# Optimization experiments

Hardware: AMD Instinct MI355X
Metric: run time of the kernel (lower is better)

Reference implementation:

```python
import jax, jax.numpy as jnp
import numpy as np

N = 100000   # nodes
E = 1600000  # edges
G = 1024     # graphs
V = 51       # attr_dims[0]+1 embedding rows (padding_idx=0)
EMB = 32
H = 2        # heads
D = 64       # hidden_dim (per-head out channels)
DC = H * D   # 128 = dim_conv
NEG_GAT = 0.2   # PyG GATConv default negative_slope
NEG_ACT = 0.05  # module's leaky_relu slope
LN_EPS = 1e-5


def setup_inputs() -> dict:
    key = jax.random.key(0)
    ks = jax.random.split(key, 20)
    def nrm(k, shape, scale=0.1):
        return jax.random.normal(k, shape, dtype=jnp.float32) * scale
    x = jax.random.randint(ks[0], (N, 1), 0, V)
    edge_index = jax.random.randint(ks[1], (2, E), 0, N)
    batch_idx = jnp.sort(jax.random.randint(ks[2], (N,), 0, G))
    return {
        'x': x, 'edge_index': edge_index, 'batch_idx': batch_idx,
        'emb': nrm(ks[3], (V, EMB)).at[0].set(0.0),  # padding_idx=0
        'ln_g': jnp.ones((EMB,), jnp.float32), 'ln_b': jnp.zeros((EMB,), jnp.float32),
        'W1': nrm(ks[4], (EMB, DC)), 'a_src1': nrm(ks[5], (H, D)), 'a_dst1': nrm(ks[6], (H, D)), 'b1': nrm(ks[7], (DC,)),
        'W2': nrm(ks[8], (DC, DC)), 'a_src2': nrm(ks[9], (H, D)), 'a_dst2': nrm(ks[10], (H, D)), 'b2': nrm(ks[11], (DC,)),
        'gw1': nrm(ks[12], (DC, D)), 'gb1': nrm(ks[13], (D,)),
        'gw2': nrm(ks[14], (D, 1)), 'gb2': nrm(ks[15], (1,)),
    }


def _gat_conv(xf, src, dst, W, a_src, a_dst, b):
    # xf: [N, in]; returns [N, H*D]. PyG GATConv, eval mode (attn dropout off).
    xw = (xf @ W).reshape(N, H, D)                           # [N,H,D]
    al_s = jnp.einsum('nhd,hd->nh', xw, a_src)
    al_d = jnp.einsum('nhd,hd->nh', xw, a_dst)
    e = jax.nn.leaky_relu(al_s[src] + al_d[dst], NEG_GAT)    # [E',H]
    m = jax.ops.segment_max(e, dst, num_segments=N)
    ex = jnp.exp(e - m[dst])
    s = jax.ops.segment_sum(ex, dst, num_segments=N)
    alpha = ex / s[dst]                                      # segment softmax over incoming edges
    msg = xw[src] * alpha[:, :, None]                        # [E',H,D]
    out = jax.ops.segment_sum(msg, dst, num_segments=N)      # [N,H,D]
    return out.reshape(N, DC) + b


def reference(x, edge_index, batch_idx, emb, ln_g, ln_b,
              W1, a_src1, a_dst1, b1, W2, a_src2, a_dst2, b2,
              gw1, gb1, gw2, gb2):
    # embedding + LayerNorm (dropout off in eval)
    xe = emb[x[:, 0]]                                        # [N,32]
    mu = jnp.mean(xe, axis=-1, keepdims=True)
    var = jnp.var(xe, axis=-1, keepdims=True)
    xe = (xe - mu) * jax.lax.rsqrt(var + LN_EPS) * ln_g + ln_b
    # add self loops (GATConv add_self_loops=True)
    ar = jnp.arange(N, dtype=edge_index.dtype)
    src = jnp.concatenate([edge_index[0], ar])
    dst = jnp.concatenate([edge_index[1], ar])
    h = jax.nn.leaky_relu(_gat_conv(xe, src, dst, W1, a_src1, a_dst1, b1), NEG_ACT)
    h = _gat_conv(h, src, dst, W2, a_src2, a_dst2, b2)       # [N,128]
    # attentional aggregation over graphs
    gate = jax.nn.leaky_relu(h @ gw1 + gb1, NEG_ACT) @ gw2 + gb2   # [N,1]
    gm = jax.ops.segment_max(gate, batch_idx, num_segments=G)
    ge = jnp.exp(gate - gm[batch_idx])
    gs = jax.ops.segment_sum(ge, batch_idx, num_segments=G)
    w = ge / gs[batch_idx]
    z = jax.ops.segment_sum(w * h, batch_idx, num_segments=G)      # [G,128]
    return h, z
```

## Files before the change

kernel.cpp:

```cpp
#include <hip/hip_runtime.h>
#include <hip/hip_bf16.h>
#include <stdint.h>

typedef unsigned short u16;
typedef unsigned int   u32;
typedef __attribute__((ext_vector_type(8))) short bf16x8;
typedef __attribute__((ext_vector_type(4))) float f32x4;

#define NEG_GAT 0.2f
#define NEG_ACT 0.05f
#define LN_EPS  1e-5f
#define NPARAM  15

__device__ __forceinline__ float bf2f(u32 bits16){
  union { u32 u; float f; } v; v.u = bits16 << 16; return v.f;
}
__device__ __forceinline__ u16 f2bf(float f){
  union { float f; u32 u; } v; v.f = f;
  u32 u = v.u;
  u32 r = (u + 0x7fffu + ((u >> 16) & 1u)) >> 16;
  return (u16)r;
}
__device__ __forceinline__ float lrelu(float x, float s){ return fmaxf(x, s * x); }

__device__ __forceinline__ int geti(const int* __restrict__ p, int i, int enc){
  return p[enc ? (2 * i) : i];
}


struct CvtParams {
  const void* src[NPARAM];
  float*      dst[NPARAM];
  int         n[NPARAM];
};

#define MAXB  2048

__global__ void k_detect(const u32* __restrict__ ln_g_raw, const int* __restrict__ ei_raw,
                         int* __restrict__ flags, int* __restrict__ bcnt)
{
  const int t = threadIdx.x;
  for (int i = t; i < MAXB; i += 256) bcnt[i] = 0;
  if (t == 0){
    flags[0] = (ln_g_raw[0] == 0x3F800000u) ? 0 : 1;
    int zeros = 0;
    for (int j = 0; j < 64; j++) if (ei_raw[2 * j + 1] == 0) zeros++;
    flags[1] = (zeros >= 60) ? 1 : 0;
    flags[2] = 0;
    flags[3] = 0;
  }
}

__global__ void k_convert(CvtParams P, const int* __restrict__ flag)
{
  const int pi  = blockIdx.y;
  const int idx = blockIdx.x * 256 + threadIdx.x;
  if (idx >= P.n[pi]) return;
  if (*flag == 0) P.dst[pi][idx] = ((const float*)P.src[pi])[idx];
  else            P.dst[pi][idx] = bf2f(((const u16*)P.src[pi])[idx]);
}


__global__ void k_checks(const int* __restrict__ batch, const int* __restrict__ x,
                         const int* __restrict__ iflag,
                         int n, int V, int* __restrict__ errflag)
{
  int i = blockIdx.x * 256 + threadIdx.x;
  const int enc = *iflag;
  if (i < n){
    int v = geti(x, i, enc);
    if ((unsigned)v >= (unsigned)V) atomicOr(errflag, 16);
    if (i < n - 1 && geti(batch, i, enc) > geti(batch, i + 1, enc)) atomicOr(errflag, 8);
  }
}

__global__ void k_check_edges(const int* __restrict__ ei, const int* __restrict__ iflag,
                              int E, int n, int* __restrict__ errflag)
{
  int e = blockIdx.x * 256 + threadIdx.x;
  if (e < E){
    int enc = *iflag;
    int s = geti(ei, e, enc);
    int d = geti(ei, E + e, enc);
    if ((unsigned)s >= (unsigned)n || (unsigned)d >= (unsigned)n) atomicOr(errflag, 32);
  }
}


__global__ void k_hist(const int* __restrict__ ei, const int* __restrict__ iflag,
                       int* __restrict__ counts, int E, int n)
{
  int e = blockIdx.x * 256 + threadIdx.x;
  if (e < E){
    int d = geti(ei, E + e, *iflag);
    d = min(max(d, 0), n - 1);
    atomicAdd(&counts[d], 1);
  }
}

__global__ void k_scanA(const int* __restrict__ counts, int* __restrict__ rowptr,
                        int* __restrict__ bsums, int n)
{
  __shared__ int sd[1024];
  int tid = threadIdx.x;
  int gid = blockIdx.x * 1024 + tid;
  int v = (gid < n) ? counts[gid] : 0;
  sd[tid] = v;
  __syncthreads();
  for (int off = 1; off < 1024; off <<= 1){
    int t = 0;
    if (tid >= off) t = sd[tid - off];
    __syncthreads();
    if (tid >= off) sd[tid] += t;
    __syncthreads();
  }
  if (gid < n) rowptr[gid] = sd[tid] - v;
  if (tid == 1023) bsums[blockIdx.x] = sd[1023];
}

__global__ void k_scanB(const int* __restrict__ bsums, int* __restrict__ boffs, int nb)
{
  __shared__ int sd[128];
  int tid = threadIdx.x;
  int v = (tid < nb) ? bsums[tid] : 0;
  sd[tid] = v;
  __syncthreads();
  for (int off = 1; off < 128; off <<= 1){
    int t = 0;
    if (tid >= off) t = sd[tid - off];
    __syncthreads();
    if (tid >= off) sd[tid] += t;
    __syncthreads();
  }
  if (tid < nb) boffs[tid] = sd[tid] - v;
}

__global__ void k_scanC(int* __restrict__ rowptr, const int* __restrict__ boffs,
                        int* __restrict__ cursor, int n, int Etot)
{
  int gid = blockIdx.x * 1024 + threadIdx.x;
  if (gid < n){
    int v = rowptr[gid] + boffs[blockIdx.x];
    rowptr[gid] = v;
    cursor[gid] = v;
  }
  if (gid == 0) rowptr[n] = Etot;
}

__global__ void k_scatter(const int* __restrict__ ei, const int* __restrict__ iflag,
                          int* __restrict__ cursor, int* __restrict__ csr, int E, int n)
{
  int e = blockIdx.x * 256 + threadIdx.x;
  if (e < E){
    int enc = *iflag;
    int s = geti(ei, e, enc);
    int d = geti(ei, E + e, enc);
    d = min(max(d, 0), n - 1);
    int pos = atomicAdd(&cursor[d], 1);
    csr[pos] = s;
  }
}

__global__ void k_check_rows(const int* __restrict__ rowptr, const int* __restrict__ cursor,
                             int n, int* __restrict__ errflag)
{
  int i = blockIdx.x * 256 + threadIdx.x;
  if (i < n){
    if (cursor[i] != rowptr[i + 1]) atomicOr(errflag, 1);
    if (i == 0 && rowptr[0] != 0)   atomicOr(errflag, 4);
  }
}

__global__ void k_check_csr(const int* __restrict__ csr, int E, int n, int* __restrict__ errflag)
{
  int e = blockIdx.x * 256 + threadIdx.x;
  if (e < E && (unsigned)csr[e] >= (unsigned)n) atomicOr(errflag, 2);
}


#define BSH   9
#define BSZ   512
#define BMSK  511
#define BINB  8192
#define BTH   512

__global__ void k_bhist(const int* __restrict__ ei, const int* __restrict__ iflag,
                        int* __restrict__ bcnt, int E, int N, int nbuck)
{
  __shared__ int h[MAXB];
  const int t = threadIdx.x;
  for (int i = t; i < nbuck; i += 256) h[i] = 0;
  __syncthreads();
  const int enc = *iflag;
  for (int e = blockIdx.x * 256 + t; e < E; e += gridDim.x * 256){
    int d = geti(ei, E + e, enc);
    d = min(max(d, 0), N - 1);
    atomicAdd(&h[d >> BSH], 1);
  }
  __syncthreads();
  for (int i = t; i < nbuck; i += 256){
    int c = h[i];
    if (c) atomicAdd(&bcnt[i], c);
  }
}

__global__ void k_bscan(const int* __restrict__ bcnt, int* __restrict__ boff,
                        int* __restrict__ gcur, int* __restrict__ rowptr,
                        int nbuck, int N, int E)
{
  __shared__ int sd[MAXB];
  const int lane = threadIdx.x;
  for (int i = lane; i < nbuck; i += 64) sd[i] = bcnt[i];
  __syncthreads();
  const int L = (nbuck + 63) >> 6;
  const int b0 = lane * L;
  int sum = 0;
  for (int j = 0; j < L; j++){ int idx = b0 + j; if (idx < nbuck) sum += sd[idx]; }
  int excl = sum;
  for (int off = 1; off < 64; off <<= 1){
    int x = __shfl_up(excl, off);
    if (lane >= off) excl += x;
  }
  excl -= sum;
  int run = excl;
  for (int j = 0; j < L; j++){
    int idx = b0 + j;
    if (idx < nbuck){ boff[idx] = run; gcur[idx] = run; run += sd[idx]; }
  }
  if (lane == 0){ boff[nbuck] = E; rowptr[N] = E; }
}

__global__ __launch_bounds__(BTH) void k_bbin(
    const int* __restrict__ ei, const int* __restrict__ iflag,
    int* __restrict__ gcur, u32* __restrict__ binned,
    int E, int N, int nbuck, int* __restrict__ errflag)
{
  __shared__ u32 stage[BINB];
  __shared__ u16 sbk[BINB];
  __shared__ int hist[MAXB];
  __shared__ int base[MAXB];
  __shared__ int gpos[MAXB];
  const int t   = threadIdx.x;
  const int e0  = blockIdx.x * BINB;
  const int cnt = min(BINB, E - e0);
  const int enc = *iflag;

  for (int i = t; i < nbuck; i += BTH) hist[i] = 0;
  __syncthreads();

  u32 pv[16]; int bk[16]; int rk[16];
  int bad = 0;
  #pragma unroll
  for (int k = 0; k < 16; k++){
    bk[k] = -1;
    int lo = k * BTH + t;
    if (lo < cnt){
      int e = e0 + lo;
      int s = geti(ei, e, enc);
      int d = geti(ei, E + e, enc);
      if ((unsigned)s >= (unsigned)N || (unsigned)d >= (unsigned)N) bad = 1;
      s = min(max(s, 0), N - 1);
      d = min(max(d, 0), N - 1);
      int b = d >> BSH;
      pv[k] = ((u32)s << BSH) | (u32)(d & BMSK);
      bk[k] = b;
      rk[k] = atomicAdd(&hist[b], 1);
    }
  }
  if (bad) atomicOr(errflag, 32);
  __syncthreads();

  if (t < 64){
    const int L = (nbuck + 63) >> 6;
    const int b0 = t * L;
    int sum = 0;
    for (int j = 0; j < L; j++){ int idx = b0 + j; if (idx < nbuck) sum += hist[idx]; }
    int excl = sum;
    for (int off = 1; off < 64; off <<= 1){
      int x = __shfl_up(excl, off);
      if (t >= off) excl += x;
    }
    excl -= sum;
    int run = excl;
    for (int j = 0; j < L; j++){
      int idx = b0 + j;
      if (idx < nbuck){ base[idx] = run; run += hist[idx]; }
    }
  }
  __syncthreads();

  for (int i = t; i < nbuck; i += BTH){
    int c = hist[i];
    gpos[i] = c ? atomicAdd(&gcur[i], c) : 0;
  }
  __syncthreads();

  #pragma unroll
  for (int k = 0; k < 16; k++){
    if (bk[k] >= 0){
      int slot = base[bk[k]] + rk[k];
      stage[slot] = pv[k];
      sbk[slot]   = (u16)bk[k];
    }
  }
  __syncthreads();

  for (int j = t; j < cnt; j += BTH){
    int b = sbk[j];
    binned[gpos[b] + (j - base[b])] = stage[j];
  }
}

__global__ __launch_bounds__(256) void k_bcsr(
    const u32* __restrict__ binned, const int* __restrict__ boff,
    int* __restrict__ rowptr, int* __restrict__ csr, int N, int nbuck)
{
  __shared__ int cnt[BSZ];
  __shared__ int rp[BSZ];
  __shared__ int cur[BSZ];
  const int b = blockIdx.x;
  const int t = threadIdx.x;
  const int lo = boff[b], hi = boff[b + 1];

  for (int i = t; i < BSZ; i += 256){ cnt[i] = 0; cur[i] = 0; }
  __syncthreads();

  for (int j = lo + t; j < hi; j += 256)
    atomicAdd(&cnt[binned[j] & BMSK], 1);
  __syncthreads();

  if (t < 64){
    const int b0 = t * 8;
    int sum = 0;
    #pragma unroll
    for (int j = 0; j < 8; j++) sum += cnt[b0 + j];
    int excl = sum;
    for (int off = 1; off < 64; off <<= 1){
      int x = __shfl_up(excl, off);
      if (t >= off) excl += x;
    }
    excl -= sum;
    int run = excl;
    #pragma unroll
    for (int j = 0; j < 8; j++){ rp[b0 + j] = run; run += cnt[b0 + j]; }
  }
  __syncthreads();

  const int node0 = b << BSH;
  for (int i = t; i < BSZ; i += 256){
    int node = node0 + i;
    if (node < N) rowptr[node] = lo + rp[i];
  }

  for (int j = lo + t; j < hi; j += 256){
    u32 pvv = binned[j];
    int dl  = pvv & BMSK;
    int pos = lo + rp[dl] + atomicAdd(&cur[dl], 1);
    csr[pos] = (int)(pvv >> BSH);
  }
}


__global__ void k_stamp_if(const int* __restrict__ errflag, float* __restrict__ out, int nel)
{
  int f = *errflag;
  if (f == 0) return;
  float s = 500.0f + 100.0f * (float)f;
  int i = blockIdx.x * 256 + threadIdx.x;
  if (i < nel) out[i] = s;
}

__global__ void k_stamp(float* __restrict__ out, int nel, float val)
{
  int i = blockIdx.x * 256 + threadIdx.x;
  if (i < nel) out[i] = val;
}


__global__ __launch_bounds__(128) void k_tables(
    const float* __restrict__ emb,
    const float* __restrict__ ln_g, const float* __restrict__ ln_b,
    const float* __restrict__ W1, const float* __restrict__ a_src,
    const float* __restrict__ a_dst,
    const float* __restrict__ W2, const float* __restrict__ gw1,
    int V,
    u16* __restrict__ xwv, float* __restrict__ alsv, float* __restrict__ aldv,
    u16* __restrict__ pb2, u16* __restrict__ pbg)
{
  const int bid = blockIdx.x;
  const int t   = threadIdx.x;

  if (bid >= V){
    if (t >= 64) return;
    int pw = bid - V;
    const float* W; int ncols, ntiles, blk; u16* pb;
    if (pw < 32){ W = W2; ncols = 128; ntiles = 8; blk = pw;      pb = pb2; }
    else        { W = gw1; ncols = 64;  ntiles = 4; blk = pw - 32; pb = pbg; }
    const int ktile = blk / ntiles;
    const int ntile = blk % ntiles;
    const int n  = ntile * 16 + (t & 15);
    const int k0 = ktile * 32 + (t >> 4) * 8;
    u16* dst = pb + ((size_t)blk * 64 + t) * 8;
    #pragma unroll
    for (int j = 0; j < 8; j++)
      dst[j] = f2bf(W[(k0 + j) * ncols + n]);
    return;
  }

  __shared__ float se[32];
  __shared__ float stats[2];
  __shared__ float sxw[128];
  const int v = bid;
  if (t < 32) se[t] = emb[v * 32 + t];
  __syncthreads();
  if (t == 0){
    float s1 = 0.f, s2 = 0.f;
    for (int k = 0; k < 32; k++){ s1 += se[k]; s2 += se[k] * se[k]; }
    float mu = s1 * (1.f / 32.f);
    float var = s2 * (1.f / 32.f) - mu * mu;
    stats[0] = mu; stats[1] = rsqrtf(var + LN_EPS);
  }
  __syncthreads();
  const float mu = stats[0], rs = stats[1];
  float o = 0.f;
  for (int k = 0; k < 32; k++){
    float xe = (se[k] - mu) * rs * ln_g[k] + ln_b[k];
    o += xe * W1[k * 128 + t];
  }
  sxw[t] = o;
  xwv[v * 128 + t] = f2bf(o);
  __syncthreads();
  if (t < 2){
    float ps = 0.f, pd = 0.f;
    for (int d = 0; d < 64; d++){
      float vv = sxw[t * 64 + d];
      ps += vv * a_src[t * 64 + d];
      pd += vv * a_dst[t * 64 + d];
    }
    alsv[2 * v + t] = ps;
    aldv[2 * v + t] = pd;
  }
}


__global__ __launch_bounds__(256, 4) void k_gatw1(
    const int* __restrict__ rowptr, const int* __restrict__ csr,
    const int* __restrict__ x, const int* __restrict__ iflag,
    const float* __restrict__ alsv, const float* __restrict__ aldv,
    const u16* __restrict__ xwv, const float* __restrict__ bias,
    int N, int V, float* __restrict__ out)
{
  extern __shared__ char smem[];
  u16*    sxwv  = (u16*)smem;
  float2* sals  = (float2*)(smem + (size_t)V * 256);
  float2* sald  = sals + V;
  float4* sedge = (float4*)(smem + (size_t)V * 256 + (size_t)V * 16);

  const int tid = threadIdx.x;
  const int enc = *iflag;

  {
    const uint4* gx = (const uint4*)xwv;
    uint4* lx = (uint4*)sxwv;
    for (int idx = tid; idx < V * 16; idx += 256) lx[idx] = gx[idx];
    const float2* ga = (const float2*)alsv;
    const float2* gd = (const float2*)aldv;
    for (int idx = tid; idx < V; idx += 256){ sals[idx] = ga[idx]; sald[idx] = gd[idx]; }
  }
  __syncthreads();

  const int wave = tid >> 6;
  const int lane = tid & 63;
  const int sub  = lane >> 4;
  const int c16  = lane & 15;
  float4* mst = sedge + wave * 64;

  for (int i = blockIdx.x * 4 + wave; i < N; i += gridDim.x * 4){
    const int r0 = rowptr[i], deg = rowptr[i + 1] - r0, total = deg + 1;
    int vi = geti(x, i, enc); vi = min(max(vi, 0), V - 1);
    const float2 ad = sald[vi];

    float sum0 = 0.f, sum1 = 0.f;
    float acc[8];
    #pragma unroll
    for (int r = 0; r < 8; r++) acc[r] = 0.f;

    if (total <= 64){
      int vs = vi;
      float a0 = -3.0e38f, a1 = -3.0e38f;
      if (lane < total){
        int s = (lane < deg) ? csr[r0 + lane] : i;
        int v = geti(x, s, enc);
        vs = min(max(v, 0), V - 1);
        float2 as = sals[vs];
        a0 = lrelu(as.x + ad.x, NEG_GAT);
        a1 = lrelu(as.y + ad.y, NEG_GAT);
      }
      float m0 = a0, m1 = a1;
      #pragma unroll
      for (int off = 32; off; off >>= 1){
        m0 = fmaxf(m0, __shfl_xor(m0, off));
        m1 = fmaxf(m1, __shfl_xor(m1, off));
      }
      float ex0 = 0.f, ex1 = 0.f;
      if (lane < total){ ex0 = __expf(a0 - m0); ex1 = __expf(a1 - m1); }
      sum0 = ex0; sum1 = ex1;
      mst[lane] = make_float4(__int_as_float(vs), ex0, ex1, 0.f);
      int qmax = (total + 3) & ~3;
      for (int q = 0; q < qmax; q += 4){
        float4 md = mst[q + sub];
        int   vj = __float_as_int(md.x);
        float ej = (c16 < 8) ? md.y : md.z;
        uint4 w = *(const uint4*)(sxwv + vj * 128 + c16 * 8);
        acc[0] += ej * bf2f(w.x & 0xffffu); acc[1] += ej * bf2f(w.x >> 16);
        acc[2] += ej * bf2f(w.y & 0xffffu); acc[3] += ej * bf2f(w.y >> 16);
        acc[4] += ej * bf2f(w.z & 0xffffu); acc[5] += ej * bf2f(w.z >> 16);
        acc[6] += ej * bf2f(w.w & 0xffffu); acc[7] += ej * bf2f(w.w >> 16);
      }
    } else {
      float m0 = -3.0e38f, m1 = -3.0e38f;
      for (int k = lane; k < total; k += 64){
        int s = (k < deg) ? csr[r0 + k] : i;
        int v = geti(x, s, enc); v = min(max(v, 0), V - 1);
        float2 as = sals[v];
        m0 = fmaxf(m0, lrelu(as.x + ad.x, NEG_GAT));
        m1 = fmaxf(m1, lrelu(as.y + ad.y, NEG_GAT));
      }
      #pragma unroll
      for (int off = 32; off; off >>= 1){
        m0 = fmaxf(m0, __shfl_xor(m0, off));
        m1 = fmaxf(m1, __shfl_xor(m1, off));
      }
      for (int base = 0; base < total; base += 64){
        int k = base + lane;
        int vs = vi; float ex0 = 0.f, ex1 = 0.f;
        if (k < total){
          int s = (k < deg) ? csr[r0 + k] : i;
          int v = geti(x, s, enc); vs = min(max(v, 0), V - 1);
          float2 as = sals[vs];
          ex0 = __expf(lrelu(as.x + ad.x, NEG_GAT) - m0);
          ex1 = __expf(lrelu(as.y + ad.y, NEG_GAT) - m1);
        }
        sum0 += ex0; sum1 += ex1;
        mst[lane] = make_float4(__int_as_float(vs), ex0, ex1, 0.f);
        int cnt = min(64, total - base);
        int qmax = (cnt + 3) & ~3;
        for (int q = 0; q < qmax; q += 4){
          float4 md = mst[q + sub];
          int   vj = __float_as_int(md.x);
          float ej = (c16 < 8) ? md.y : md.z;
          uint4 w = *(const uint4*)(sxwv + vj * 128 + c16 * 8);
          acc[0] += ej * bf2f(w.x & 0xffffu); acc[1] += ej * bf2f(w.x >> 16);
          acc[2] += ej * bf2f(w.y & 0xffffu); acc[3] += ej * bf2f(w.y >> 16);
          acc[4] += ej * bf2f(w.z & 0xffffu); acc[5] += ej * bf2f(w.z >> 16);
          acc[6] += ej * bf2f(w.w & 0xffffu); acc[7] += ej * bf2f(w.w >> 16);
        }
      }
    }

    #pragma unroll
    for (int off = 32; off; off >>= 1){
      sum0 += __shfl_xor(sum0, off);
      sum1 += __shfl_xor(sum1, off);
    }
    #pragma unroll
    for (int r = 0; r < 8; r++){
      acc[r] += __shfl_xor(acc[r], 16);
      acc[r] += __shfl_xor(acc[r], 32);
    }

    if (sub == 0){
      float inv = 1.f / ((c16 < 8) ? sum0 : sum1);
      const float4* bp = (const float4*)(bias + c16 * 8);
      float4 b0 = bp[0], b1 = bp[1];
      float4 o0, o1;
      o0.x = lrelu(acc[0] * inv + b0.x, NEG_ACT); o0.y = lrelu(acc[1] * inv + b0.y, NEG_ACT);
      o0.z = lrelu(acc[2] * inv + b0.z, NEG_ACT); o0.w = lrelu(acc[3] * inv + b0.w, NEG_ACT);
      o1.x = lrelu(acc[4] * inv + b1.x, NEG_ACT); o1.y = lrelu(acc[5] * inv + b1.y, NEG_ACT);
      o1.z = lrelu(acc[6] * inv + b1.z, NEG_ACT); o1.w = lrelu(acc[7] * inv + b1.w, NEG_ACT);
      float* op = out + (size_t)i * 128 + c16 * 8;
      *(float4*)op       = o0;
      *(float4*)(op + 4) = o1;
    }
  }
}

__global__ __launch_bounds__(64, 8) void k_gatw1g(
    const int* __restrict__ rowptr, const int* __restrict__ csr,
    const int* __restrict__ x, const int* __restrict__ iflag,
    const float* __restrict__ alsv, const float* __restrict__ aldv,
    const u16* __restrict__ xwv, const float* __restrict__ bias,
    int V, float* __restrict__ out)
{
  const int i    = blockIdx.x;
  const int lane = threadIdx.x;
  const int sub  = lane >> 4;
  const int c16  = lane & 15;
  const int enc  = *iflag;
  const int r0 = rowptr[i], deg = rowptr[i + 1] - r0, total = deg + 1;
  int vi = geti(x, i, enc); vi = min(max(vi, 0), V - 1);
  const float ad0 = aldv[2 * vi], ad1 = aldv[2 * vi + 1];

  float sum0 = 0.f, sum1 = 0.f;
  float acc[8];
  #pragma unroll
  for (int r = 0; r < 8; r++) acc[r] = 0.f;

  float m0 = -3.0e38f, m1 = -3.0e38f;
  for (int k = lane; k < total; k += 64){
    int s = (k < deg) ? csr[r0 + k] : i;
    int v = geti(x, s, enc); v = min(max(v, 0), V - 1);
    float2 as = *(const float2*)(alsv + 2 * v);
    m0 = fmaxf(m0, lrelu(as.x + ad0, NEG_GAT));
    m1 = fmaxf(m1, lrelu(as.y + ad1, NEG_GAT));
  }
  #pragma unroll
  for (int off = 32; off; off >>= 1){
    m0 = fmaxf(m0, __shfl_xor(m0, off));
    m1 = fmaxf(m1, __shfl_xor(m1, off));
  }
  for (int base = 0; base < total; base += 64){
    int k = base + lane;
    int vs = vi; float ex0 = 0.f, ex1 = 0.f;
    if (k < total){
      int s = (k < deg) ? csr[r0 + k] : i;
      int v = geti(x, s, enc); vs = min(max(v, 0), V - 1);
      float2 as = *(const float2*)(alsv + 2 * vs);
      ex0 = __expf(lrelu(as.x + ad0, NEG_GAT) - m0);
      ex1 = __expf(lrelu(as.y + ad1, NEG_GAT) - m1);
    }
    sum0 += ex0; sum1 += ex1;
    int cnt = min(64, total - base);
    int qmax = (cnt + 3) & ~3;
    for (int q = 0; q < qmax; q += 4){
      int   j  = q + sub;
      int   vj = __shfl(vs, j);
      float e0 = __shfl(ex0, j);
      float e1 = __shfl(ex1, j);
      float ej = (c16 < 8) ? e0 : e1;
      uint4 w = *(const uint4*)(xwv + (size_t)vj * 128 + c16 * 8);
      acc[0] += ej * bf2f(w.x & 0xffffu); acc[1] += ej * bf2f(w.x >> 16);
      acc[2] += ej * bf2f(w.y & 0xffffu); acc[3] += ej * bf2f(w.y >> 16);
      acc[4] += ej * bf2f(w.z & 0xffffu); acc[5] += ej * bf2f(w.z >> 16);
      acc[6] += ej * bf2f(w.w & 0xffffu); acc[7] += ej * bf2f(w.w >> 16);
    }
  }

  #pragma unroll
  for (int off = 32; off; off >>= 1){
    sum0 += __shfl_xor(sum0, off);
    sum1 += __shfl_xor(sum1, off);
  }
  #pragma unroll
  for (int r = 0; r < 8; r++){
    acc[r] += __shfl_xor(acc[r], 16);
    acc[r] += __shfl_xor(acc[r], 32);
  }

  if (sub == 0){
    float inv = 1.f / ((c16 < 8) ? sum0 : sum1);
    const float4* bp = (const float4*)(bias + c16 * 8);
    float4 b0 = bp[0], b1 = bp[1];
    float4 o0, o1;
    o0.x = lrelu(acc[0] * inv + b0.x, NEG_ACT); o0.y = lrelu(acc[1] * inv + b0.y, NEG_ACT);
    o0.z = lrelu(acc[2] * inv + b0.z, NEG_ACT); o0.w = lrelu(acc[3] * inv + b0.w, NEG_ACT);
    o1.x = lrelu(acc[4] * inv + b1.x, NEG_ACT); o1.y = lrelu(acc[5] * inv + b1.y, NEG_ACT);
    o1.z = lrelu(acc[6] * inv + b1.z, NEG_ACT); o1.w = lrelu(acc[7] * inv + b1.w, NEG_ACT);
    float* op = out + (size_t)i * 128 + c16 * 8;
    *(float4*)op       = o0;
    *(float4*)(op + 4) = o1;
  }
}


__global__ __launch_bounds__(64, 8) void k_gatw2(
    const int* __restrict__ rowptr, const int* __restrict__ csr,
    const float* __restrict__ al_s, const float* __restrict__ al_d,
    const u16* __restrict__ xw, const float* __restrict__ bias,
    int apply_act, float* __restrict__ out)
{
  const int i    = blockIdx.x;
  const int lane = threadIdx.x;
  const int sub  = lane >> 4;
  const int c16  = lane & 15;
  const int r0 = rowptr[i], deg = rowptr[i + 1] - r0, total = deg + 1;
  const float2 ad = *(const float2*)(al_d + 2 * i);

  float sum0 = 0.f, sum1 = 0.f;
  float acc[8];
  #pragma unroll
  for (int r = 0; r < 8; r++) acc[r] = 0.f;

  if (total <= 64){
    int s = i;
    float a0 = -3.0e38f, a1 = -3.0e38f;
    if (lane < total){
      s = (lane < deg) ? csr[r0 + lane] : i;
      float2 as = *(const float2*)(al_s + 2 * s);
      a0 = lrelu(as.x + ad.x, NEG_GAT);
      a1 = lrelu(as.y + ad.y, NEG_GAT);
    }
    float m0 = a0, m1 = a1;
    #pragma unroll
    for (int off = 32; off; off >>= 1){
      m0 = fmaxf(m0, __shfl_xor(m0, off));
      m1 = fmaxf(m1, __shfl_xor(m1, off));
    }
    float ex0 = 0.f, ex1 = 0.f;
    if (lane < total){ ex0 = __expf(a0 - m0); ex1 = __expf(a1 - m1); }
    sum0 = ex0; sum1 = ex1;
    int qmax = (total + 3) & ~3;
    for (int q = 0; q < qmax; q += 4){
      int   j  = q + sub;
      int   sj = __shfl(s, j);
      float e0 = __shfl(ex0, j);
      float e1 = __shfl(ex1, j);
      float ej = (c16 < 8) ? e0 : e1;
      uint4 w = *(const uint4*)(xw + (size_t)sj * 128 + c16 * 8);
      acc[0] += ej * bf2f(w.x & 0xffffu); acc[1] += ej * bf2f(w.x >> 16);
      acc[2] += ej * bf2f(w.y & 0xffffu); acc[3] += ej * bf2f(w.y >> 16);
      acc[4] += ej * bf2f(w.z & 0xffffu); acc[5] += ej * bf2f(w.z >> 16);
      acc[6] += ej * bf2f(w.w & 0xffffu); acc[7] += ej * bf2f(w.w >> 16);
    }
  } else {
    float m0 = -3.0e38f, m1 = -3.0e38f;
    for (int k = lane; k < total; k += 64){
      int s = (k < deg) ? csr[r0 + k] : i;
      float2 as = *(const float2*)(al_s + 2 * s);
      m0 = fmaxf(m0, lrelu(as.x + ad.x, NEG_GAT));
      m1 = fmaxf(m1, lrelu(as.y + ad.y, NEG_GAT));
    }
    #pragma unroll
    for (int off = 32; off; off >>= 1){
      m0 = fmaxf(m0, __shfl_xor(m0, off));
      m1 = fmaxf(m1, __shfl_xor(m1, off));
    }
    for (int base = 0; base < total; base += 64){
      int k = base + lane;
      int s = i; float ex0 = 0.f, ex1 = 0.f;
      if (k < total){
        s = (k < deg) ? csr[r0 + k] : i;
        float2 as = *(const float2*)(al_s + 2 * s);
        ex0 = __expf(lrelu(as.x + ad.x, NEG_GAT) - m0);
        ex1 = __expf(lrelu(as.y + ad.y, NEG_GAT) - m1);
      }
      sum0 += ex0; sum1 += ex1;
      int cnt = min(64, total - base);
      int qmax = (cnt + 3) & ~3;
      for (int q = 0; q < qmax; q += 4){
        int   j  = q + sub;
        int   sj = __shfl(s, j);
        float e0 = __shfl(ex0, j);
        float e1 = __shfl(ex1, j);
        float ej = (c16 < 8) ? e0 : e1;
        uint4 w = *(const uint4*)(xw + (size_t)sj * 128 + c16 * 8);
        acc[0] += ej * bf2f(w.x & 0xffffu); acc[1] += ej * bf2f(w.x >> 16);
        acc[2] += ej * bf2f(w.y & 0xffffu); acc[3] += ej * bf2f(w.y >> 16);
        acc[4] += ej * bf2f(w.z & 0xffffu); acc[5] += ej * bf2f(w.z >> 16);
        acc[6] += ej * bf2f(w.w & 0xffffu); acc[7] += ej * bf2f(w.w >> 16);
      }
    }
  }

  #pragma unroll
  for (int off = 32; off; off >>= 1){
    sum0 += __shfl_xor(sum0, off);
    sum1 += __shfl_xor(sum1, off);
  }
  #pragma unroll
  for (int r = 0; r < 8; r++){
    acc[r] += __shfl_xor(acc[r], 16);
    acc[r] += __shfl_xor(acc[r], 32);
  }

  if (sub == 0){
    float inv = 1.f / ((c16 < 8) ? sum0 : sum1);
    const float4* bp = (const float4*)(bias + c16 * 8);
    float4 b0 = bp[0], b1 = bp[1];
    float4 o0, o1;
    o0.x = acc[0] * inv + b0.x; o0.y = acc[1] * inv + b0.y;
    o0.z = acc[2] * inv + b0.z; o0.w = acc[3] * inv + b0.w;
    o1.x = acc[4] * inv + b1.x; o1.y = acc[5] * inv + b1.y;
    o1.z = acc[6] * inv + b1.z; o1.w = acc[7] * inv + b1.w;
    if (apply_act){
      o0.x = lrelu(o0.x, NEG_ACT); o0.y = lrelu(o0.y, NEG_ACT);
      o0.z = lrelu(o0.z, NEG_ACT); o0.w = lrelu(o0.w, NEG_ACT);
      o1.x = lrelu(o1.x, NEG_ACT); o1.y = lrelu(o1.y, NEG_ACT);
      o1.z = lrelu(o1.z, NEG_ACT); o1.w = lrelu(o1.w, NEG_ACT);
    }
    float* op = out + (size_t)i * 128 + c16 * 8;
    *(float4*)op       = o0;
    *(float4*)(op + 4) = o1;
  }
}


__global__ __launch_bounds__(256, 2) void k_node2m(
    const float* __restrict__ h1, const u16* __restrict__ pb2,
    const float* __restrict__ a_src, const float* __restrict__ a_dst,
    int N, u16* __restrict__ xw, float* __restrict__ al_s, float* __restrict__ al_d)
{
  const int wave = threadIdx.x >> 6;
  const int lane = threadIdx.x & 63;
  const int rowbase = blockIdx.x * 64 + wave * 16;
  const int m    = lane & 15;
  const int quad = lane >> 4;

  int arow = rowbase + m; if (arow >= N) arow = N - 1;
  const float* aptr = h1 + (size_t)arow * 128 + quad * 8;

  f32x4 acc[8];
  #pragma unroll
  for (int nt = 0; nt < 8; nt++) acc[nt] = (f32x4){0.f, 0.f, 0.f, 0.f};

  #pragma unroll
  for (int kt = 0; kt < 4; kt++){
    float4 a0 = *(const float4*)(aptr + kt * 32);
    float4 a1 = *(const float4*)(aptr + kt * 32 + 4);
    bf16x8 af;
    af[0] = (short)f2bf(a0.x); af[1] = (short)f2bf(a0.y);
    af[2] = (short)f2bf(a0.z); af[3] = (short)f2bf(a0.w);
    af[4] = (short)f2bf(a1.x); af[5] = (short)f2bf(a1.y);
    af[6] = (short)f2bf(a1.z); af[7] = (short)f2bf(a1.w);
    const u16* bbase = pb2 + (((size_t)kt * 8) * 64 + lane) * 8;
    #pragma unroll
    for (int nt = 0; nt < 8; nt++){
      bf16x8 bf = *(const bf16x8*)(bbase + (size_t)nt * 64 * 8);
      acc[nt] = __builtin_amdgcn_mfma_f32_16x16x32_bf16(af, bf, acc[nt], 0, 0, 0);
    }
  }

  float asv[8], adv[8];
  #pragma unroll
  for (int nt = 0; nt < 8; nt++){
    asv[nt] = a_src[nt * 16 + m];
    adv[nt] = a_dst[nt * 16 + m];
  }
  #pragma unroll
  for (int r = 0; r < 4; r++){
    int row = rowbase + quad * 4 + r;
    bool ok = row < N;
    float s0 = 0.f, s1 = 0.f, d0 = 0.f, d1 = 0.f;
    #pragma unroll
    for (int nt = 0; nt < 8; nt++){
      float v = acc[nt][r];
      if (ok) xw[(size_t)row * 128 + nt * 16 + m] = f2bf(v);
      if (nt < 4){ s0 += v * asv[nt]; d0 += v * adv[nt]; }
      else       { s1 += v * asv[nt]; d1 += v * adv[nt]; }
    }
    #pragma unroll
    for (int off = 1; off < 16; off <<= 1){
      s0 += __shfl_xor(s0, off); s1 += __shfl_xor(s1, off);
      d0 += __shfl_xor(d0, off); d1 += __shfl_xor(d1, off);
    }
    if (ok && m == 0){
      al_s[2 * row] = s0; al_s[2 * row + 1] = s1;
      al_d[2 * row] = d0; al_d[2 * row + 1] = d1;
    }
  }
}


__global__ __launch_bounds__(256, 2) void k_gatem(
    const float* __restrict__ h, const u16* __restrict__ pbg,
    const float* __restrict__ gb1, const float* __restrict__ gw2,
    const float* __restrict__ gb2, int N, float* __restrict__ gate)
{
  const int wave = threadIdx.x >> 6;
  const int lane = threadIdx.x & 63;
  const int rowbase = blockIdx.x * 64 + wave * 16;
  const int m    = lane & 15;
  const int quad = lane >> 4;

  int arow = rowbase + m; if (arow >= N) arow = N - 1;
  const float* aptr = h + (size_t)arow * 128 + quad * 8;

  f32x4 acc[4];
  #pragma unroll
  for (int nt = 0; nt < 4; nt++) acc[nt] = (f32x4){0.f, 0.f, 0.f, 0.f};

  #pragma unroll
  for (int kt = 0; kt < 4; kt++){
    float4 a0 = *(const float4*)(aptr + kt * 32);
    float4 a1 = *(const float4*)(aptr + kt * 32 + 4);
    bf16x8 af;
    af[0] = (short)f2bf(a0.x); af[1] = (short)f2bf(a0.y);
    af[2] = (short)f2bf(a0.z); af[3] = (short)f2bf(a0.w);
    af[4] = (short)f2bf(a1.x); af[5] = (short)f2bf(a1.y);
    af[6] = (short)f2bf(a1.z); af[7] = (short)f2bf(a1.w);
    const u16* bbase = pbg + (((size_t)kt * 4) * 64 + lane) * 8;
    #pragma unroll
    for (int nt = 0; nt < 4; nt++){
      bf16x8 bf = *(const bf16x8*)(bbase + (size_t)nt * 64 * 8);
      acc[nt] = __builtin_amdgcn_mfma_f32_16x16x32_bf16(af, bf, acc[nt], 0, 0, 0);
    }
  }

  float gbv[4], g2v[4];
  #pragma unroll
  for (int nt = 0; nt < 4; nt++){
    gbv[nt] = gb1[nt * 16 + m];
    g2v[nt] = gw2[nt * 16 + m];
  }
  const float g2b = gb2[0];
  #pragma unroll
  for (int r = 0; r < 4; r++){
    int row = rowbase + quad * 4 + r;
    float q = 0.f;
    #pragma unroll
    for (int nt = 0; nt < 4; nt++)
      q += lrelu(acc[nt][r] + gbv[nt], NEG_ACT) * g2v[nt];
    #pragma unroll
    for (int off = 1; off < 16; off <<= 1) q += __shfl_xor(q, off);
    if (row < N && m == 0) gate[row] = q + g2b;
  }
}


__global__ __launch_bounds__(256) void k_graphsw(
    const int* __restrict__ batch, const int* __restrict__ iflag,
    const float* __restrict__ gate,
    const float* __restrict__ h, float* __restrict__ zout, int N)
{
  __shared__ int   range[2];
  __shared__ float red[8];
  __shared__ float sz[128];
  const int g = blockIdx.x, t = threadIdx.x;
  const int wave = t >> 6, lane = t & 63;
  if (t == 0){
    const int enc = *iflag;
    int lo = 0, hi = N;
    while (lo < hi){ int mid = (lo + hi) >> 1; if (geti(batch, mid, enc) < g) lo = mid + 1; else hi = mid; }
    range[0] = lo;
    hi = N;
    while (lo < hi){ int mid = (lo + hi) >> 1; if (geti(batch, mid, enc) < g + 1) lo = mid + 1; else hi = mid; }
    range[1] = lo;
  }
  __syncthreads();
  const int st = range[0], en = range[1];

  float m = -3.0e38f;
  for (int k = st + t; k < en; k += 256) m = fmaxf(m, gate[k]);
  #pragma unroll
  for (int off = 32; off; off >>= 1) m = fmaxf(m, __shfl_xor(m, off));
  if (lane == 0) red[wave] = m;
  __syncthreads();
  m = fmaxf(fmaxf(red[0], red[1]), fmaxf(red[2], red[3]));

  float s = 0.f;
  for (int k = st + t; k < en; k += 256) s += __expf(gate[k] - m);
  #pragma unroll
  for (int off = 32; off; off >>= 1) s += __shfl_xor(s, off);
  if (lane == 0) red[4 + wave] = s;
  __syncthreads();
  s = (red[4] + red[5]) + (red[6] + red[7]);

  const float inv = 1.f / s;
  const int half = t >> 7, t2 = t & 127;
  float z = 0.f;
  for (int k = st + half; k < en; k += 2){
    float wk = __expf(gate[k] - m) * inv;
    z += wk * h[(size_t)k * 128 + t2];
  }
  if (half == 1) sz[t2] = z;
  __syncthreads();
  if (half == 0) zout[(size_t)g * 128 + t2] = z + sz[t2];
}


extern "C" void kernel_launch(void* const* d_in, const int* in_sizes, int n_in,
                              void* d_out, int out_size, void* d_ws, size_t ws_size,
                              hipStream_t stream)
{
  const int* x      = (const int*)d_in[0];
  const int* ei     = (const int*)d_in[1];
  const int* batch  = (const int*)d_in[2];

  const int N = in_sizes[0];
  const int E = in_sizes[1] / 2;
  const int V = in_sizes[3] / 32;
  const int G = out_size / 128 - N;

  char* p = (char*)d_ws;
  auto alloc = [&](size_t bytes) -> char* {
    char* r = p; p += (bytes + 255) & ~(size_t)255; return r;
  };
  int*   multi  = (int*)  alloc((size_t)N * 4);
  int*   rowptr = (int*)  alloc((size_t)(N + 1) * 4);
  int*   csr    = (int*)  alloc((size_t)E * 4);
  int*   bsums  = (int*)  alloc(4096);
  int*   boffs  = (int*)  alloc(4096);
  int*   flags  = (int*)  alloc(256);
  int*   fflag  = flags;
  int*   iflag  = flags + 1;
  int*   errflg = flags + 2;
  float* al_s   = (float*)alloc((size_t)N * 2 * 4);
  float* al_d   = (float*)alloc((size_t)N * 2 * 4);
  u16*   xw     = (u16*)  alloc((size_t)N * 128 * 2);
  u16*   xwv    = (u16*)  alloc((size_t)V * 128 * 2);
  float* alsv   = (float*)alloc((size_t)V * 2 * 4);
  float* aldv   = (float*)alloc((size_t)V * 2 * 4);
  u16*   pb2    = (u16*)  alloc((size_t)128 * 128 * 2);
  u16*   pbg    = (u16*)  alloc((size_t)128 * 64 * 2);

  const int nbuck = (N + BSZ - 1) >> BSH;
  int*   bcnt   = (int*)  alloc((size_t)(MAXB) * 4);
  int*   boff   = (int*)  alloc((size_t)(MAXB + 1) * 4);
  int*   gcur   = (int*)  alloc((size_t)(MAXB) * 4);
  u32*   binned = (u32*)  alloc((size_t)E * 4);

  CvtParams cp;
  float* fpar[NPARAM];
  int maxn = 0;
  for (int pi = 0; pi < NPARAM; pi++){
    int n = in_sizes[3 + pi];
    fpar[pi] = (float*)alloc((size_t)n * 4);
    cp.src[pi] = d_in[3 + pi];
    cp.dst[pi] = fpar[pi];
    cp.n[pi]   = n;
    if (n > maxn) maxn = n;
  }
  const size_t needed = (size_t)(p - (char*)d_ws);

  const float* emb    = fpar[0];
  const float* ln_g   = fpar[1];
  const float* ln_b   = fpar[2];
  const float* W1     = fpar[3];
  const float* a_src1 = fpar[4];
  const float* a_dst1 = fpar[5];
  const float* b1     = fpar[6];
  const float* W2     = fpar[7];
  const float* a_src2 = fpar[8];
  const float* a_dst2 = fpar[9];
  const float* b2     = fpar[10];
  const float* gw1    = fpar[11];
  const float* gb1    = fpar[12];
  const float* gw2    = fpar[13];
  const float* gb2    = fpar[14];
  (void)n_in;

  int ob = (out_size + 255) / 256;
  if (ws_size < needed){
    k_stamp<<<ob, 256, 0, stream>>>((float*)d_out, out_size, 9999.0f);
    return;
  }

  int*   counts = multi;
  int*   cursor = multi;
  float* gate   = (float*)multi;
  float* hbuf   = (float*)d_out;
  float* zbuf   = (float*)d_out + (size_t)N * 128;

  k_detect<<<1, 256, 0, stream>>>((const u32*)d_in[4], ei, flags, bcnt);
  dim3 cgrid((maxn + 255) / 256, NPARAM);
  k_convert<<<cgrid, 256, 0, stream>>>(cp, fflag);

  int eb = (E + 255) / 256;
  int nb = (N + 1023) / 1024;
  int nb256 = (N + 255) / 256;

  k_checks<<<nb256, 256, 0, stream>>>(batch, x, iflag, N, V, errflg);

  if (nbuck <= MAXB){
    k_bhist<<<256, 256, 0, stream>>>(ei, iflag, bcnt, E, N, nbuck);
    k_bscan<<<1, 64, 0, stream>>>(bcnt, boff, gcur, rowptr, nbuck, N, E);
    k_bbin<<<(E + BINB - 1) / BINB, BTH, 0, stream>>>(ei, iflag, gcur, binned, E, N, nbuck, errflg);
    k_bcsr<<<nbuck, 256, 0, stream>>>(binned, boff, rowptr, csr, N, nbuck);
  } else {
    k_check_edges<<<eb, 256, 0, stream>>>(ei, iflag, E, N, errflg);
    hipMemsetAsync(counts, 0, (size_t)N * 4, stream);
    hipMemsetAsync(csr, 0xFF, (size_t)E * 4, stream);
    k_hist<<<eb, 256, 0, stream>>>(ei, iflag, counts, E, N);
    k_scanA<<<nb, 1024, 0, stream>>>(counts, rowptr, bsums, N);
    k_scanB<<<1, 128, 0, stream>>>(bsums, boffs, nb);
    k_scanC<<<nb, 1024, 0, stream>>>(rowptr, boffs, cursor, N, E);
    k_scatter<<<eb, 256, 0, stream>>>(ei, iflag, cursor, csr, E, N);
    k_check_rows<<<nb256, 256, 0, stream>>>(rowptr, cursor, N, errflg);
    k_check_csr<<<eb, 256, 0, stream>>>(csr, E, N, errflg);
  }

  k_tables<<<V + 48, 128, 0, stream>>>(emb, ln_g, ln_b, W1, a_src1, a_dst1,
                                       W2, gw1, V, xwv, alsv, aldv, pb2, pbg);

  const int gwb = min(2048, (N + 3) / 4);
  const size_t smem1 = (size_t)V * 272 + 4096;
  if (smem1 <= 64 * 1024){
    k_gatw1<<<gwb, 256, smem1, stream>>>(rowptr, csr, x, iflag, alsv, aldv, xwv, b1, N, V, hbuf);
  } else {
    k_gatw1g<<<N, 64, 0, stream>>>(rowptr, csr, x, iflag, alsv, aldv, xwv, b1, V, hbuf);
  }

  const int gblk = (N + 63) / 64;
  k_node2m<<<gblk, 256, 0, stream>>>(hbuf, pb2, a_src2, a_dst2, N, xw, al_s, al_d);

  k_gatw2<<<N, 64, 0, stream>>>(rowptr, csr, al_s, al_d, xw, b2, 0, hbuf);

  k_gatem<<<gblk, 256, 0, stream>>>(hbuf, pbg, gb1, gw2, gb2, N, gate);
  k_graphsw<<<G, 256, 0, stream>>>(batch, iflag, gate, hbuf, zbuf, N);

  k_stamp_if<<<ob, 256, 0, stream>>>(errflg, (float*)d_out, out_size);
}
```

Before: 375.7 us.

## Store layer-1 activations as bf16, widen graph pooling blocks, grid-stride stamp kernels

The first GAT layer now writes its output as packed bf16 into a separate buffer, and the second-layer projection reads bf16 directly instead of loading fp32 and converting. This halves the write and read traffic for the intermediate activations. The graph pooling kernel moves to 512 threads with a four-way split over nodes and an extra shared-memory reduction. The error-stamp kernels become grid-stride loops with a fixed grid of 512 blocks, so far fewer blocks launch when there is no error.

```diff
diff --git a/kernel.cpp b/kernel.cpp
--- a/kernel.cpp
+++ b/kernel.cpp
@@ -366,14 +366,12 @@
   int f = *errflag;
   if (f == 0) return;
   float s = 500.0f + 100.0f * (float)f;
-  int i = blockIdx.x * 256 + threadIdx.x;
-  if (i < nel) out[i] = s;
+  for (int i = blockIdx.x * 256 + threadIdx.x; i < nel; i += gridDim.x * 256) out[i] = s;
 }
 
 __global__ void k_stamp(float* __restrict__ out, int nel, float val)
 {
-  int i = blockIdx.x * 256 + threadIdx.x;
-  if (i < nel) out[i] = val;
+  for (int i = blockIdx.x * 256 + threadIdx.x; i < nel; i += gridDim.x * 256) out[i] = val;
 }
 
 
@@ -448,7 +446,7 @@
     const int* __restrict__ x, const int* __restrict__ iflag,
     const float* __restrict__ alsv, const float* __restrict__ aldv,
     const u16* __restrict__ xwv, const float* __restrict__ bias,
-    int N, int V, float* __restrict__ out)
+    int N, int V, u16* __restrict__ out)
 {
   extern __shared__ char smem[];
   u16*    sxwv  = (u16*)smem;
@@ -573,14 +571,17 @@
       float inv = 1.f / ((c16 < 8) ? sum0 : sum1);
       const float4* bp = (const float4*)(bias + c16 * 8);
       float4 b0 = bp[0], b1 = bp[1];
-      float4 o0, o1;
-      o0.x = lrelu(acc[0] * inv + b0.x, NEG_ACT); o0.y = lrelu(acc[1] * inv + b0.y, NEG_ACT);
-      o0.z = lrelu(acc[2] * inv + b0.z, NEG_ACT); o0.w = lrelu(acc[3] * inv + b0.w, NEG_ACT);
-      o1.x = lrelu(acc[4] * inv + b1.x, NEG_ACT); o1.y = lrelu(acc[5] * inv + b1.y, NEG_ACT);
-      o1.z = lrelu(acc[6] * inv + b1.z, NEG_ACT); o1.w = lrelu(acc[7] * inv + b1.w, NEG_ACT);
-      float* op = out + (size_t)i * 128 + c16 * 8;
-      *(float4*)op       = o0;
-      *(float4*)(op + 4) = o1;
+      float o[8];
+      o[0] = lrelu(acc[0] * inv + b0.x, NEG_ACT); o[1] = lrelu(acc[1] * inv + b0.y, NEG_ACT);
+      o[2] = lrelu(acc[2] * inv + b0.z, NEG_ACT); o[3] = lrelu(acc[3] * inv + b0.w, NEG_ACT);
+      o[4] = lrelu(acc[4] * inv + b1.x, NEG_ACT); o[5] = lrelu(acc[5] * inv + b1.y, NEG_ACT);
+      o[6] = lrelu(acc[6] * inv + b1.z, NEG_ACT); o[7] = lrelu(acc[7] * inv + b1.w, NEG_ACT);
+      uint4 pk;
+      pk.x = (u32)f2bf(o[0]) | ((u32)f2bf(o[1]) << 16);
+      pk.y = (u32)f2bf(o[2]) | ((u32)f2bf(o[3]) << 16);
+      pk.z = (u32)f2bf(o[4]) | ((u32)f2bf(o[5]) << 16);
+      pk.w = (u32)f2bf(o[6]) | ((u32)f2bf(o[7]) << 16);
+      *(uint4*)(out + (size_t)i * 128 + c16 * 8) = pk;
     }
   }
 }
@@ -590,7 +591,7 @@
     const int* __restrict__ x, const int* __restrict__ iflag,
     const float* __restrict__ alsv, const float* __restrict__ aldv,
     const u16* __restrict__ xwv, const float* __restrict__ bias,
-    int V, float* __restrict__ out)
+    int V, u16* __restrict__ out)
 {
   const int i    = blockIdx.x;
   const int lane = threadIdx.x;
@@ -661,14 +662,17 @@
     float inv = 1.f / ((c16 < 8) ? sum0 : sum1);
     const float4* bp = (const float4*)(bias + c16 * 8);
     float4 b0 = bp[0], b1 = bp[1];
-    float4 o0, o1;
-    o0.x = lrelu(acc[0] * inv + b0.x, NEG_ACT); o0.y = lrelu(acc[1] * inv + b0.y, NEG_ACT);
-    o0.z = lrelu(acc[2] * inv + b0.z, NEG_ACT); o0.w = lrelu(acc[3] * inv + b0.w, NEG_ACT);
-    o1.x = lrelu(acc[4] * inv + b1.x, NEG_ACT); o1.y = lrelu(acc[5] * inv + b1.y, NEG_ACT);
-    o1.z = lrelu(acc[6] * inv + b1.z, NEG_ACT); o1.w = lrelu(acc[7] * inv + b1.w, NEG_ACT);
-    float* op = out + (size_t)i * 128 + c16 * 8;
-    *(float4*)op       = o0;
-    *(float4*)(op + 4) = o1;
+    float o[8];
+    o[0] = lrelu(acc[0] * inv + b0.x, NEG_ACT); o[1] = lrelu(acc[1] * inv + b0.y, NEG_ACT);
+    o[2] = lrelu(acc[2] * inv + b0.z, NEG_ACT); o[3] = lrelu(acc[3] * inv + b0.w, NEG_ACT);
+    o[4] = lrelu(acc[4] * inv + b1.x, NEG_ACT); o[5] = lrelu(acc[5] * inv + b1.y, NEG_ACT);
+    o[6] = lrelu(acc[6] * inv + b1.z, NEG_ACT); o[7] = lrelu(acc[7] * inv + b1.w, NEG_ACT);
+    uint4 pk;
+    pk.x = (u32)f2bf(o[0]) | ((u32)f2bf(o[1]) << 16);
+    pk.y = (u32)f2bf(o[2]) | ((u32)f2bf(o[3]) << 16);
+    pk.z = (u32)f2bf(o[4]) | ((u32)f2bf(o[5]) << 16);
+    pk.w = (u32)f2bf(o[6]) | ((u32)f2bf(o[7]) << 16);
+    *(uint4*)(out + (size_t)i * 128 + c16 * 8) = pk;
   }
 }
 
@@ -796,7 +800,7 @@
 
 
 __global__ __launch_bounds__(256, 2) void k_node2m(
-    const float* __restrict__ h1, const u16* __restrict__ pb2,
+    const u16* __restrict__ h1b, const u16* __restrict__ pb2,
     const float* __restrict__ a_src, const float* __restrict__ a_dst,
     int N, u16* __restrict__ xw, float* __restrict__ al_s, float* __restrict__ al_d)
 {
@@ -807,7 +811,7 @@
   const int quad = lane >> 4;
 
   int arow = rowbase + m; if (arow >= N) arow = N - 1;
-  const float* aptr = h1 + (size_t)arow * 128 + quad * 8;
+  const u16* aptr = h1b + (size_t)arow * 128 + quad * 8;
 
   f32x4 acc[8];
   #pragma unroll
@@ -815,13 +819,7 @@
 
   #pragma unroll
   for (int kt = 0; kt < 4; kt++){
-    float4 a0 = *(const float4*)(aptr + kt * 32);
-    float4 a1 = *(const float4*)(aptr + kt * 32 + 4);
-    bf16x8 af;
-    af[0] = (short)f2bf(a0.x); af[1] = (short)f2bf(a0.y);
-    af[2] = (short)f2bf(a0.z); af[3] = (short)f2bf(a0.w);
-    af[4] = (short)f2bf(a1.x); af[5] = (short)f2bf(a1.y);
-    af[6] = (short)f2bf(a1.z); af[7] = (short)f2bf(a1.w);
+    bf16x8 af = *(const bf16x8*)(aptr + kt * 32);
     const u16* bbase = pb2 + (((size_t)kt * 8) * 64 + lane) * 8;
     #pragma unroll
     for (int nt = 0; nt < 8; nt++){
@@ -917,14 +915,14 @@
 }
 
 
-__global__ __launch_bounds__(256) void k_graphsw(
+__global__ __launch_bounds__(512) void k_graphsw(
     const int* __restrict__ batch, const int* __restrict__ iflag,
     const float* __restrict__ gate,
     const float* __restrict__ h, float* __restrict__ zout, int N)
 {
   __shared__ int   range[2];
-  __shared__ float red[8];
-  __shared__ float sz[128];
+  __shared__ float red[16];
+  __shared__ float sz[3][128];
   const int g = blockIdx.x, t = threadIdx.x;
   const int wave = t >> 6, lane = t & 63;
   if (t == 0){
@@ -940,31 +938,35 @@
   const int st = range[0], en = range[1];
 
   float m = -3.0e38f;
-  for (int k = st + t; k < en; k += 256) m = fmaxf(m, gate[k]);
+  for (int k = st + t; k < en; k += 512) m = fmaxf(m, gate[k]);
   #pragma unroll
   for (int off = 32; off; off >>= 1) m = fmaxf(m, __shfl_xor(m, off));
   if (lane == 0) red[wave] = m;
   __syncthreads();
-  m = fmaxf(fmaxf(red[0], red[1]), fmaxf(red[2], red[3]));
+  m = red[0];
+  #pragma unroll
+  for (int w = 1; w < 8; w++) m = fmaxf(m, red[w]);
 
   float s = 0.f;
-  for (int k = st + t; k < en; k += 256) s += __expf(gate[k] - m);
+  for (int k = st + t; k < en; k += 512) s += __expf(gate[k] - m);
   #pragma unroll
   for (int off = 32; off; off >>= 1) s += __shfl_xor(s, off);
-  if (lane == 0) red[4 + wave] = s;
-  __syncthreads();
-  s = (red[4] + red[5]) + (red[6] + red[7]);
+  if (lane == 0) red[8 + wave] = s;
+  __syncthreads();
+  s = red[8];
+  #pragma unroll
+  for (int w = 9; w < 16; w++) s += red[w];
 
   const float inv = 1.f / s;
-  const int half = t >> 7, t2 = t & 127;
+  const int quarter = t >> 7, t2 = t & 127;
   float z = 0.f;
-  for (int k = st + half; k < en; k += 2){
+  for (int k = st + quarter; k < en; k += 4){
     float wk = __expf(gate[k] - m) * inv;
     z += wk * h[(size_t)k * 128 + t2];
   }
-  if (half == 1) sz[t2] = z;
-  __syncthreads();
-  if (half == 0) zout[(size_t)g * 128 + t2] = z + sz[t2];
+  if (quarter) sz[quarter - 1][t2] = z;
+  __syncthreads();
+  if (quarter == 0) zout[(size_t)g * 128 + t2] = z + sz[0][t2] + sz[1][t2] + sz[2][t2];
 }
 
 
@@ -997,6 +999,7 @@
   float* al_s   = (float*)alloc((size_t)N * 2 * 4);
   float* al_d   = (float*)alloc((size_t)N * 2 * 4);
   u16*   xw     = (u16*)  alloc((size_t)N * 128 * 2);
+  u16*   h1b    = (u16*)  alloc((size_t)N * 128 * 2);
   u16*   xwv    = (u16*)  alloc((size_t)V * 128 * 2);
   float* alsv   = (float*)alloc((size_t)V * 2 * 4);
   float* aldv   = (float*)alloc((size_t)V * 2 * 4);
@@ -1039,9 +1042,8 @@
   const float* gb2    = fpar[14];
   (void)n_in;
 
-  int ob = (out_size + 255) / 256;
   if (ws_size < needed){
-    k_stamp<<<ob, 256, 0, stream>>>((float*)d_out, out_size, 9999.0f);
+    k_stamp<<<512, 256, 0, stream>>>((float*)d_out, out_size, 9999.0f);
     return;
   }
 
@@ -1085,18 +1087,18 @@
   const int gwb = min(2048, (N + 3) / 4);
   const size_t smem1 = (size_t)V * 272 + 4096;
   if (smem1 <= 64 * 1024){
-    k_gatw1<<<gwb, 256, smem1, stream>>>(rowptr, csr, x, iflag, alsv, aldv, xwv, b1, N, V, hbuf);
+    k_gatw1<<<gwb, 256, smem1, stream>>>(rowptr, csr, x, iflag, alsv, aldv, xwv, b1, N, V, h1b);
   } else {
-    k_gatw1g<<<N, 64, 0, stream>>>(rowptr, csr, x, iflag, alsv, aldv, xwv, b1, V, hbuf);
+    k_gatw1g<<<N, 64, 0, stream>>>(rowptr, csr, x, iflag, alsv, aldv, xwv, b1, V, h1b);
   }
 
   const int gblk = (N + 63) / 64;
-  k_node2m<<<gblk, 256, 0, stream>>>(hbuf, pb2, a_src2, a_dst2, N, xw, al_s, al_d);
+  k_node2m<<<gblk, 256, 0, stream>>>(h1b, pb2, a_src2, a_dst2, N, xw, al_s, al_d);
 
   k_gatw2<<<N, 64, 0, stream>>>(rowptr, csr, al_s, al_d, xw, b2, 0, hbuf);
 
   k_gatem<<<gblk, 256, 0, stream>>>(hbuf, pbg, gb1, gw2, gb2, N, gate);
-  k_graphsw<<<G, 256, 0, stream>>>(batch, iflag, gate, hbuf, zbuf, N);
-
-  k_stamp_if<<<ob, 256, 0, stream>>>(errflg, (float*)d_out, out_size);
-}
+  k_graphsw<<<G, 512, 0, stream>>>(batch, iflag, gate, hbuf, zbuf, N);
+
+  k_stamp_if<<<512, 256, 0, stream>>>(errflg, (float*)d_out, out_size);
+}
```

Measured after the change: 352.6 us. -6.2%, faster.
